# Optimization experiments

Hardware: AMD Instinct MI355X
Metric: run time of the kernel (lower is better)

The kernel has to match this reference:

```python
import jax, jax.numpy as jnp
import numpy as np

NUM_CLASSES = 100000
NUM_SAMPLED = 1000
DIM = 512
BATCH = 8192


def _log_uniform_expected_count(ids, num_sampled, range_max):
    # TF LogUniformCandidateSampler: p(c) = (log(c+2) - log(c+1)) / log(range_max+1)
    c = ids.astype(jnp.float32)
    p = (jnp.log(c + 2.0) - jnp.log(c + 1.0)) / jnp.log(float(range_max) + 1.0)
    # expected count under unique sampling with num_sampled tries
    return -jnp.expm1(num_sampled * jnp.log1p(-p))


def setup_inputs() -> dict:
    key = jax.random.key(0)
    k1, k2, k3, k4, k5 = jax.random.split(key, 5)
    y_true = jax.random.randint(k1, (BATCH, 1), 0, NUM_CLASSES, dtype=jnp.int32)
    y_pred = jax.random.normal(k2, (BATCH, DIM), dtype=jnp.float32)
    # learned params sized per init_kwargs (VarianceScaling ~ small uniform; scale only)
    limit = np.sqrt(6.0 / (NUM_CLASSES + DIM))
    W = jax.random.uniform(k3, (NUM_CLASSES, DIM), jnp.float32, -limit, limit)
    b = jax.random.uniform(k4, (NUM_CLASSES,), jnp.float32, -limit, limit)
    sampled = jax.random.randint(k5, (NUM_SAMPLED,), 0, NUM_CLASSES, dtype=jnp.int32)
    return {"y_true": y_true, "y_pred": y_pred, "W": W, "b": b, "sampled": sampled}


def reference(y_true, y_pred, W, b, sampled):
    V = W.shape[0]
    S = sampled.shape[0]
    labels = y_true[:, 0]  # [B], num_true = 1

    # true-class logits: gather rows + batched dot
    w_true = W[labels]                                      # [B, D]
    true_logits = jnp.einsum('bd,bd->b', y_pred, w_true) + b[labels]
    true_logits = true_logits - jnp.log(_log_uniform_expected_count(labels, S, V))

    # sampled-class logits: gather rows + GEMM
    w_s = W[sampled]                                        # [S, D]
    sampled_logits = y_pred @ w_s.T + b[sampled]            # [B, S]
    sampled_logits = sampled_logits - jnp.log(_log_uniform_expected_count(sampled, S, V))

    # remove accidental hits (sampled id == true label)
    hit = labels[:, None] == sampled[None, :]               # [B, S]
    sampled_logits = jnp.where(hit, sampled_logits - 1e9, sampled_logits)

    # softmax cross-entropy with true class at column 0
    logits = jnp.concatenate([true_logits[:, None], sampled_logits], axis=1)  # [B, S+1]
    per_example = jax.nn.logsumexp(logits, axis=1) - logits[:, 0]
    return jnp.mean(per_example)
```

## Files before the change

### kernel.cpp

```cpp
#include <hip/hip_runtime.h>
#include <hip/hip_bf16.h>
#include <math.h>

#define S_SAMPLED 1000
#define SPAD      1024
#define DIM       512
#define BATCH     8192

#define BM 128
#define BN 128
#define BKT 64
#define KTILES (DIM / BKT)
#define NCHUNK 8
#define GEMM_BLOCKS 512
#define M0C 20.0f

typedef __attribute__((ext_vector_type(8))) short short8_t;
typedef __attribute__((ext_vector_type(4))) float f32x4_t;

__device__ __forceinline__ float neg_log_expected(int c) {
    const float log_vp1 = 11.5129354649f;
    float p = log1pf(1.0f / (float)(c + 1)) / log_vp1;
    float E = -expm1f((float)S_SAMPLED * log1pf(-p));
    return -logf(E);
}

__device__ __forceinline__ unsigned short f2bf(float x) {
    __hip_bfloat16 h = __float2bfloat16(x);
    union { __hip_bfloat16 h; unsigned short u; } cv; cv.h = h; return cv.u;
}

__device__ __forceinline__ void load_lds16(const void* g, void* l) {
    __builtin_amdgcn_global_load_lds(
        (const __attribute__((address_space(1))) void*)g,
        (__attribute__((address_space(3))) void*)l, 16, 0, 0);
}

__device__ __forceinline__ int swz(int lin) { return lin ^ (((lin >> 7) & 7) << 4); }

__global__ __launch_bounds__(256) void prep_kernel(
    const int* __restrict__ y_true, const float* __restrict__ y_pred,
    const float* __restrict__ W, const float* __restrict__ b,
    const int* __restrict__ sampled,
    unsigned short* __restrict__ Wg, float* __restrict__ adj,
    float* __restrict__ true_out, unsigned short* __restrict__ ypredB)
{
    int bid = blockIdx.x;
    if (bid < 512) {
        int row = bid * 2 + (threadIdx.x >> 7);
        int t   = threadIdx.x & 127;
        if (t == 0) {
            if (row < S_SAMPLED) {
                int c = sampled[row];
                adj[row] = b[c] + neg_log_expected(c);
            } else adj[row] = -1e30f;
        }
        unsigned short* dst = Wg + (size_t)row * DIM + t * 4;
        if (row < S_SAMPLED) {
            float4 f = *(const float4*)(W + (size_t)sampled[row] * DIM + t * 4);
            ushort4 o;
            o.x = f2bf(f.x); o.y = f2bf(f.y); o.z = f2bf(f.z); o.w = f2bf(f.w);
            *(ushort4*)dst = o;
        } else {
            *(ushort4*)dst = make_ushort4(0, 0, 0, 0);
        }
    } else {
        int row  = (bid - 512) * 4 + (threadIdx.x >> 6);
        int lane = threadIdx.x & 63;
        int lab  = y_true[row];
        const float4* ap = (const float4*)(y_pred + (size_t)row * DIM);
        const float4* wp = (const float4*)(W + (size_t)lab * DIM);
        float s = 0.f;
#pragma unroll
        for (int u = 0; u < 2; ++u) {
            float4 a = ap[lane + u * 64];
            float4 w = wp[lane + u * 64];
            s += a.x * w.x + a.y * w.y + a.z * w.z + a.w * w.w;
            ushort4 o;
            o.x = f2bf(a.x); o.y = f2bf(a.y); o.z = f2bf(a.z); o.w = f2bf(a.w);
            *(ushort4*)(ypredB + (size_t)row * DIM + (lane + u * 64) * 4) = o;
        }
#pragma unroll
        for (int off = 32; off; off >>= 1) s += __shfl_xor(s, off);
        if (lane == 0) true_out[row] = s + b[lab] + neg_log_expected(lab);
    }
}

__global__ __launch_bounds__(512, 4) void gemm_partial_kernel(
    const unsigned short* __restrict__ Abf,
    const unsigned short* __restrict__ Wg,
    const int*   __restrict__ sampled,
    const float* __restrict__ adj,
    const int*   __restrict__ y_true,
    float*       __restrict__ psum)
{
    __shared__ __align__(16) char smem[65536 + 1024];
    char* As0 = smem;
    char* As1 = smem + 16384;
    char* Bs0 = smem + 32768;
    char* Bs1 = smem + 49152;
    float* reds = (float*)(smem + 65536);

    int wg = blockIdx.x;
    int sw = (wg & 7) * 64 + (wg >> 3);
    const int m0    = (sw >> 3) * BM;
    const int chunk = sw & 7;
    const int n0    = chunk * BN;

    const int tid  = threadIdx.x;
    const int lane = tid & 63;
    const int wid  = tid >> 6;
    const int wr   = wid >> 1;
    const int wc   = wid & 1;
    const int g    = lane >> 4;
    const int lcol = lane & 15;

    const char* AB = (const char*)Abf;
    const char* WB = (const char*)Wg;

    int a_src[2], b_src[2];
#pragma unroll
    for (int it = 0; it < 2; ++it) {
        int d = it * 8192 + tid * 16;
        int row = d >> 7;
        int kb  = (d & 127) ^ ((row & 7) << 4);
        a_src[it] = (m0 + row) * (DIM * 2) + kb;
        b_src[it] = (n0 + row) * (DIM * 2) + kb;
    }

    int a_roff[2][2], b_roff[4][2];
#pragma unroll
    for (int mi = 0; mi < 2; ++mi)
#pragma unroll
        for (int ks = 0; ks < 2; ++ks)
            a_roff[mi][ks] = swz((wr * 32 + mi * 16 + lcol) * 128 + ks * 64 + g * 16);
#pragma unroll
    for (int nj = 0; nj < 4; ++nj)
#pragma unroll
        for (int ks = 0; ks < 2; ++ks)
            b_roff[nj][ks] = swz((wc * 64 + nj * 16 + lcol) * 128 + ks * 64 + g * 16);

    f32x4_t acc[2][4] = {};

#define STAGE(AsP, BsP, kt) do {                                     \
        int kb_ = (kt) * 128;                                        \
        load_lds16(AB + a_src[0] + kb_, (AsP) + tid * 16);           \
        load_lds16(AB + a_src[1] + kb_, (AsP) + 8192 + tid * 16);    \
        load_lds16(WB + b_src[0] + kb_, (BsP) + tid * 16);           \
        load_lds16(WB + b_src[1] + kb_, (BsP) + 8192 + tid * 16);    \
    } while (0)

#define COMPUTE(AsP, BsP) do {                                                        \
        _Pragma("unroll")                                                             \
        for (int ks = 0; ks < 2; ++ks) {                                              \
            short8_t a0 = *(const short8_t*)((AsP) + a_roff[0][ks]);                  \
            short8_t a1 = *(const short8_t*)((AsP) + a_roff[1][ks]);                  \
            _Pragma("unroll")                                                         \
            for (int nj = 0; nj < 4; ++nj) {                                          \
                short8_t bv = *(const short8_t*)((BsP) + b_roff[nj][ks]);             \
                acc[0][nj] = __builtin_amdgcn_mfma_f32_16x16x32_bf16(a0, bv, acc[0][nj], 0, 0, 0); \
                acc[1][nj] = __builtin_amdgcn_mfma_f32_16x16x32_bf16(a1, bv, acc[1][nj], 0, 0, 0); \
            }                                                                         \
        }                                                                             \
    } while (0)

    __builtin_amdgcn_sched_barrier(0);
    STAGE(As0, Bs0, 0);
    STAGE(As1, Bs1, 1);
#pragma unroll
    for (int t = 0; t < KTILES; ++t) {
        if (t < KTILES - 1) asm volatile("s_waitcnt vmcnt(4)" ::: "memory");
        else                asm volatile("s_waitcnt vmcnt(0)" ::: "memory");
        __builtin_amdgcn_s_barrier();
        __builtin_amdgcn_sched_barrier(0);
        const char* AsP = (t & 1) ? As1 : As0;
        const char* BsP = (t & 1) ? Bs1 : Bs0;
        __builtin_amdgcn_s_setprio(1);
        COMPUTE(AsP, BsP);
        __builtin_amdgcn_s_setprio(0);
        __builtin_amdgcn_sched_barrier(0);
        __builtin_amdgcn_s_barrier();
        if (t + 2 < KTILES) STAGE((t & 1) ? As1 : As0, (t & 1) ? Bs1 : Bs0, t + 2);
    }
    __builtin_amdgcn_sched_barrier(0);

    int   labs[2][4];
    float srow[2][4];
#pragma unroll
    for (int mi = 0; mi < 2; ++mi)
#pragma unroll
        for (int r = 0; r < 4; ++r) {
            labs[mi][r] = y_true[m0 + wr * 32 + mi * 16 + g * 4 + r];
            srow[mi][r] = 0.f;
        }

    float ajv[4]; int scv[4];
#pragma unroll
    for (int nj = 0; nj < 4; ++nj) {
        int cg = n0 + wc * 64 + nj * 16 + lcol;
        ajv[nj] = adj[cg];
        scv[nj] = (cg < S_SAMPLED) ? sampled[cg] : -2147483647;
    }

#pragma unroll
    for (int mi = 0; mi < 2; ++mi)
#pragma unroll
        for (int nj = 0; nj < 4; ++nj) {
#pragma unroll
            for (int r = 0; r < 4; ++r) {
                float x = acc[mi][nj][r] + ajv[nj];
                if (scv[nj] == labs[mi][r]) x -= 1e9f;
                srow[mi][r] += expf(x - M0C);
            }
        }

#pragma unroll
    for (int s = 1; s < 16; s <<= 1)
#pragma unroll
        for (int mi = 0; mi < 2; ++mi)
#pragma unroll
            for (int r = 0; r < 4; ++r)
                srow[mi][r] += __shfl_xor(srow[mi][r], s);
    if (lcol == 0) {
#pragma unroll
        for (int mi = 0; mi < 2; ++mi)
#pragma unroll
            for (int r = 0; r < 4; ++r)
                reds[wc * 128 + wr * 32 + mi * 16 + g * 4 + r] = srow[mi][r];
    }
    __syncthreads();

    if (tid < BM)
        psum[(size_t)(m0 + tid) * NCHUNK + chunk] = reds[tid] + reds[128 + tid];
#undef STAGE
#undef COMPUTE
}

__global__ __launch_bounds__(1024) void finalize_kernel(
    const float* __restrict__ psum, const float* __restrict__ true_v,
    float* __restrict__ out)
{
    __shared__ float sm[1024];
    float tot = 0.f;
#pragma unroll
    for (int u = 0; u < BATCH / 1024; ++u) {
        int r = u * 1024 + threadIdx.x;
        float4 p0 = *(const float4*)(psum + (size_t)r * NCHUNK);
        float4 p1 = *(const float4*)(psum + (size_t)r * NCHUNK + 4);
        float t = true_v[r];
        float s = p0.x + p0.y + p0.z + p0.w
                + p1.x + p1.y + p1.z + p1.w + expf(t - M0C);
        tot += logf(s) + M0C - t;
    }
    sm[threadIdx.x] = tot;
    __syncthreads();
    for (int st = 512; st; st >>= 1) {
        if (threadIdx.x < st) sm[threadIdx.x] += sm[threadIdx.x + st];
        __syncthreads();
    }
    if (threadIdx.x == 0) out[0] = sm[0] / (float)BATCH;
}

extern "C" void kernel_launch(void* const* d_in, const int* in_sizes, int n_in,
                              void* d_out, int out_size, void* d_ws, size_t ws_size,
                              hipStream_t stream) {
    const int*   y_true  = (const int*)d_in[0];
    const float* y_pred  = (const float*)d_in[1];
    const float* W       = (const float*)d_in[2];
    const float* b       = (const float*)d_in[3];
    const int*   sampled = (const int*)d_in[4];

    char* ws = (char*)d_ws;
    unsigned short* ypredB = (unsigned short*)ws;
    unsigned short* Wg     = (unsigned short*)(ws + 8388608);
    float* adj    = (float*)(ws + 9437184);
    float* true_v = (float*)(ws + 9441280);
    float* psum   = (float*)(ws + 9474048);

    prep_kernel<<<2560, 256, 0, stream>>>(y_true, y_pred, W, b, sampled,
                                          Wg, adj, true_v, ypredB);
    gemm_partial_kernel<<<GEMM_BLOCKS, 512, 0, stream>>>(
        ypredB, Wg, sampled, adj, y_true, psum);
    finalize_kernel<<<1, 1024, 0, stream>>>(psum, true_v, (float*)d_out);
}
```

Measured before the change: 34.09 us.

## Move true-logit dot into GEMM epilogue and parallelize finalize across blocks

The per-row true-class gather and dot product moves from the prep kernel into the GEMM kernel's epilogue, using the bf16 copy of y_pred. Prep now only converts y_pred to bf16 with wider vector stores. The finalize reduction is split across 8 blocks, and the last block combines the partial sums via an atomic counter that prep resets. This cuts prep work and serial finalize latency, at the cost of a slightly lower-precision true logit and extra global loads in the GEMM tail.

```diff
diff --git a/kernel.cpp b/kernel.cpp
--- a/kernel.cpp
+++ b/kernel.cpp
@@ -13,6 +13,7 @@
 #define KTILES (DIM / BKT)
 #define NCHUNK 8
 #define GEMM_BLOCKS 512
+#define FIN_BLOCKS 8
 #define M0C 20.0f
 
 typedef __attribute__((ext_vector_type(8))) short short8_t;
@@ -30,6 +31,12 @@
     union { __hip_bfloat16 h; unsigned short u; } cv; cv.h = h; return cv.u;
 }
 
+__device__ __forceinline__ float b2f(short u) {
+    union { float f; unsigned u; } c;
+    c.u = ((unsigned)(unsigned short)u) << 16;
+    return c.f;
+}
+
 __device__ __forceinline__ void load_lds16(const void* g, void* l) {
     __builtin_amdgcn_global_load_lds(
         (const __attribute__((address_space(1))) void*)g,
@@ -39,13 +46,13 @@
 __device__ __forceinline__ int swz(int lin) { return lin ^ (((lin >> 7) & 7) << 4); }
 
 __global__ __launch_bounds__(256) void prep_kernel(
-    const int* __restrict__ y_true, const float* __restrict__ y_pred,
-    const float* __restrict__ W, const float* __restrict__ b,
-    const int* __restrict__ sampled,
+    const float* __restrict__ y_pred, const float* __restrict__ W,
+    const float* __restrict__ b, const int* __restrict__ sampled,
     unsigned short* __restrict__ Wg, float* __restrict__ adj,
-    float* __restrict__ true_out, unsigned short* __restrict__ ypredB)
+    unsigned short* __restrict__ ypredB, int* __restrict__ counter)
 {
     int bid = blockIdx.x;
+    if (bid == 0 && threadIdx.x == 0) *counter = 0;
     if (bid < 512) {
         int row = bid * 2 + (threadIdx.x >> 7);
         int t   = threadIdx.x & 127;
@@ -65,24 +72,15 @@
             *(ushort4*)dst = make_ushort4(0, 0, 0, 0);
         }
     } else {
-        int row  = (bid - 512) * 4 + (threadIdx.x >> 6);
-        int lane = threadIdx.x & 63;
-        int lab  = y_true[row];
-        const float4* ap = (const float4*)(y_pred + (size_t)row * DIM);
-        const float4* wp = (const float4*)(W + (size_t)lab * DIM);
-        float s = 0.f;
-#pragma unroll
-        for (int u = 0; u < 2; ++u) {
-            float4 a = ap[lane + u * 64];
-            float4 w = wp[lane + u * 64];
-            s += a.x * w.x + a.y * w.y + a.z * w.z + a.w * w.w;
-            ushort4 o;
-            o.x = f2bf(a.x); o.y = f2bf(a.y); o.z = f2bf(a.z); o.w = f2bf(a.w);
-            *(ushort4*)(ypredB + (size_t)row * DIM + (lane + u * 64) * 4) = o;
-        }
-#pragma unroll
-        for (int off = 32; off; off >>= 1) s += __shfl_xor(s, off);
-        if (lane == 0) true_out[row] = s + b[lab] + neg_log_expected(lab);
+        int i = (bid - 512) * 2048 + threadIdx.x * 8;
+        float4 f0 = *(const float4*)(y_pred + i);
+        float4 f1 = *(const float4*)(y_pred + i + 4);
+        uint4 o;
+        o.x = (unsigned)f2bf(f0.x) | ((unsigned)f2bf(f0.y) << 16);
+        o.y = (unsigned)f2bf(f0.z) | ((unsigned)f2bf(f0.w) << 16);
+        o.z = (unsigned)f2bf(f1.x) | ((unsigned)f2bf(f1.y) << 16);
+        o.w = (unsigned)f2bf(f1.z) | ((unsigned)f2bf(f1.w) << 16);
+        *(uint4*)(ypredB + i) = o;
     }
 }
 
@@ -92,6 +90,9 @@
     const int*   __restrict__ sampled,
     const float* __restrict__ adj,
     const int*   __restrict__ y_true,
+    const float* __restrict__ W,
+    const float* __restrict__ b,
+    float*       __restrict__ true_v,
     float*       __restrict__ psum)
 {
     __shared__ __align__(16) char smem[65536 + 1024];
@@ -184,6 +185,22 @@
     }
     __builtin_amdgcn_sched_barrier(0);
 
+#pragma unroll
+    for (int rr = 0; rr < 2; ++rr) {
+        int row = m0 + chunk * 16 + wid * 2 + rr;
+        int lab = y_true[row];
+        short8_t a8 = *(const short8_t*)(Abf + (size_t)row * DIM + lane * 8);
+        float4 w0 = *(const float4*)(W + (size_t)lab * DIM + lane * 8);
+        float4 w1 = *(const float4*)(W + (size_t)lab * DIM + lane * 8 + 4);
+        float s = b2f(a8[0]) * w0.x + b2f(a8[1]) * w0.y
+                + b2f(a8[2]) * w0.z + b2f(a8[3]) * w0.w
+                + b2f(a8[4]) * w1.x + b2f(a8[5]) * w1.y
+                + b2f(a8[6]) * w1.z + b2f(a8[7]) * w1.w;
+#pragma unroll
+        for (int off = 32; off; off >>= 1) s += __shfl_xor(s, off);
+        if (lane == 0) true_v[row] = s + b[lab] + neg_log_expected(lab);
+    }
+
     int   labs[2][4];
     float srow[2][4];
 #pragma unroll
@@ -238,27 +255,36 @@
 
 __global__ __launch_bounds__(1024) void finalize_kernel(
     const float* __restrict__ psum, const float* __restrict__ true_v,
+    float* __restrict__ partial, int* __restrict__ counter,
     float* __restrict__ out)
 {
     __shared__ float sm[1024];
-    float tot = 0.f;
-#pragma unroll
-    for (int u = 0; u < BATCH / 1024; ++u) {
-        int r = u * 1024 + threadIdx.x;
-        float4 p0 = *(const float4*)(psum + (size_t)r * NCHUNK);
-        float4 p1 = *(const float4*)(psum + (size_t)r * NCHUNK + 4);
-        float t = true_v[r];
-        float s = p0.x + p0.y + p0.z + p0.w
-                + p1.x + p1.y + p1.z + p1.w + expf(t - M0C);
-        tot += logf(s) + M0C - t;
-    }
-    sm[threadIdx.x] = tot;
+    __shared__ int s_last;
+    int r = blockIdx.x * 1024 + threadIdx.x;
+    float4 p0 = *(const float4*)(psum + (size_t)r * NCHUNK);
+    float4 p1 = *(const float4*)(psum + (size_t)r * NCHUNK + 4);
+    float t = true_v[r];
+    float s = p0.x + p0.y + p0.z + p0.w
+            + p1.x + p1.y + p1.z + p1.w + expf(t - M0C);
+    sm[threadIdx.x] = logf(s) + M0C - t;
     __syncthreads();
     for (int st = 512; st; st >>= 1) {
         if (threadIdx.x < st) sm[threadIdx.x] += sm[threadIdx.x + st];
         __syncthreads();
     }
-    if (threadIdx.x == 0) out[0] = sm[0] / (float)BATCH;
+    if (threadIdx.x == 0) {
+        partial[blockIdx.x] = sm[0];
+        __threadfence();
+        int old = atomicAdd(counter, 1);
+        s_last = (old == FIN_BLOCKS - 1) ? 1 : 0;
+    }
+    __syncthreads();
+    if (!s_last || threadIdx.x != 0) return;
+    __threadfence();
+    float tot = 0.f;
+#pragma unroll
+    for (int i = 0; i < FIN_BLOCKS; ++i) tot += partial[i];
+    out[0] = tot / (float)BATCH;
 }
 
 extern "C" void kernel_launch(void* const* d_in, const int* in_sizes, int n_in,
@@ -273,13 +299,16 @@
     char* ws = (char*)d_ws;
     unsigned short* ypredB = (unsigned short*)ws;
     unsigned short* Wg     = (unsigned short*)(ws + 8388608);
-    float* adj    = (float*)(ws + 9437184);
-    float* true_v = (float*)(ws + 9441280);
-    float* psum   = (float*)(ws + 9474048);
-
-    prep_kernel<<<2560, 256, 0, stream>>>(y_true, y_pred, W, b, sampled,
-                                          Wg, adj, true_v, ypredB);
+    float* adj     = (float*)(ws + 9437184);
+    float* true_v  = (float*)(ws + 9441280);
+    float* psum    = (float*)(ws + 9474048);
+    float* partial = (float*)(ws + 9736192);
+    int*   counter = (int*)(ws + 9736256);
+
+    prep_kernel<<<2560, 256, 0, stream>>>(y_pred, W, b, sampled,
+                                          Wg, adj, ypredB, counter);
     gemm_partial_kernel<<<GEMM_BLOCKS, 512, 0, stream>>>(
-        ypredB, Wg, sampled, adj, y_true, psum);
-    finalize_kernel<<<1, 1024, 0, stream>>>(psum, true_v, (float*)d_out);
-}
+        ypredB, Wg, sampled, adj, y_true, W, b, true_v, psum);
+    finalize_kernel<<<FIN_BLOCKS, 1024, 0, stream>>>(
+        psum, true_v, partial, counter, (float*)d_out);
+}
```

Measured after the change: 33.63 us. About the same (-1.4%).
